# Optimization experiments

Measured on AMD Instinct MI355X. Metric: run time of the kernel, lower is better.

Reference implementation:

```python
import jax, jax.numpy as jnp
import numpy as np

NUM_TABLES = 10
EMB_DIM = 3
VOCAB = 1_000_000
N_IDX = 4_000_000
N_BAGS = 100_000


def setup_inputs() -> dict:
    key = jax.random.key(0)
    k_idx, k_off, k_w = jax.random.split(key, 3)
    eb_input = jax.random.randint(k_idx, (N_IDX,), 0, VOCAB, dtype=jnp.int64)
    # EmbeddingBag offsets: sorted, first element must be 0, values in [0, N_IDX)
    eb_offset = jnp.sort(jax.random.randint(k_off, (N_BAGS,), 0, N_IDX, dtype=jnp.int64))
    eb_offset = eb_offset.at[0].set(0)
    # torch.nn.EmbeddingBag default init: N(0, 1)
    W = jax.random.normal(k_w, (NUM_TABLES, VOCAB, EMB_DIM), dtype=jnp.float32)
    return {"eb_input": eb_input, "eb_offset": eb_offset, "W": W}


def _bag_sums(eb_input, eb_offset, W):
    # segment id for each index position: bag b covers [offset[b], offset[b+1])
    n = eb_input.shape[0]
    seg = jnp.searchsorted(eb_offset, jnp.arange(n), side="right") - 1  # [N]
    gathered = W[:, eb_input, :]  # [T, N, D] irregular gather
    # sum-pool per bag for every table
    per_bag = jax.vmap(lambda g: jax.ops.segment_sum(g, seg, num_segments=eb_offset.shape[0]))(gathered)  # [T, B, D]
    return per_bag


def reference(eb_input, eb_offset, W):
    per_bag = _bag_sums(eb_input, eb_offset, W)  # [10, B, 3]
    outs = [per_bag[i] for i in range(NUM_TABLES)]
    outs[5] = jnp.sum(outs[5], axis=1, keepdims=True)  # [B, 1]
    outs[6] = jnp.sum(outs[6], axis=1, keepdims=True)  # [B, 1]
    cat = jnp.concatenate(outs, axis=1)  # [B, 26]
    return jnp.sum(cat, axis=0)  # [26]
```

## Files before the change

### kernel.cpp

```cpp
#include <hip/hip_runtime.h>

#define VOCAB 1000000
#define NUM_TABLES 10
#define OUT_SIZE 26
#define BUCKET_BITS 12
#define BPB 4096
#define NBUCKETS 245
#define CHUNK 16384
#define MAXSRC 256
#define GSTRIDE 256
#define NGROUPS (VOCAB / 4)
#define RBLK ((NGROUPS + 255) / 256)
#define NSERIES 30


__global__ void __launch_bounds__(1024) scatter_kernel(
    const int* __restrict__ idx, int n,
    unsigned short* __restrict__ scat,
    unsigned int* __restrict__ gs32)
{
    __shared__ unsigned int lcount[256];
    __shared__ unsigned int sc[256];
    __shared__ __align__(16) unsigned short stage[CHUNK];
    const int tid = threadIdx.x;
    if (tid < 256) lcount[tid] = 0u;
    __syncthreads();

    const int4* idx4 = (const int4*)idx;
    const int n4 = n >> 2;
    const int base4 = blockIdx.x * (CHUNK / 4);
    int4 q[4];
    bool val[4];
    unsigned rank[16];
    unsigned bkt[16];
#pragma unroll
    for (int j = 0; j < 4; ++j) {
        int i4 = base4 + j * 1024 + tid;
        val[j] = (i4 < n4);
        if (val[j]) q[j] = idx4[i4];
    }
#pragma unroll
    for (int j = 0; j < 4; ++j) {
        if (val[j]) {
            unsigned v[4] = {(unsigned)q[j].x, (unsigned)q[j].y, (unsigned)q[j].z, (unsigned)q[j].w};
#pragma unroll
            for (int e = 0; e < 4; ++e) {
                bkt[j * 4 + e] = v[e] >> BUCKET_BITS;
                rank[j * 4 + e] = atomicAdd(&lcount[bkt[j * 4 + e]], 1u);
            }
        }
    }
    unsigned trank[3], tbkt[3];
    int tcnt = 0;
    if (blockIdx.x == gridDim.x - 1 && tid == 0) {
        for (int i = n4 * 4; i < n; ++i) {
            unsigned u = (unsigned)idx[i];
            tbkt[tcnt] = u >> BUCKET_BITS;
            trank[tcnt] = atomicAdd(&lcount[tbkt[tcnt]], 1u);
            ++tcnt;
        }
    }
    __syncthreads();
    unsigned cnt = 0;
    if (tid < 256) {
        cnt = (tid < NBUCKETS) ? lcount[tid] : 0u;
        sc[tid] = cnt;
    }
    __syncthreads();
#pragma unroll
    for (int off = 1; off < 256; off <<= 1) {
        unsigned v = 0, a = 0;
        if (tid < 256) {
            v = sc[tid];
            if (tid >= off) a = sc[tid - off];
        }
        __syncthreads();
        if (tid < 256) sc[tid] = v + a;
        __syncthreads();
    }
    if (tid < 256) {
        unsigned excl = sc[tid] - cnt;
        if (tid < NBUCKETS) gs32[(size_t)blockIdx.x * GSTRIDE + tid] = excl | (cnt << 16);
        lcount[tid] = excl;
    }
    __syncthreads();
#pragma unroll
    for (int j = 0; j < 4; ++j) {
        if (val[j]) {
            unsigned v[4] = {(unsigned)q[j].x, (unsigned)q[j].y, (unsigned)q[j].z, (unsigned)q[j].w};
#pragma unroll
            for (int e = 0; e < 4; ++e) {
                unsigned k = j * 4 + e;
                stage[lcount[bkt[k]] + rank[k]] = (unsigned short)(v[e] & (BPB - 1));
            }
        }
    }
    if (blockIdx.x == gridDim.x - 1 && tid == 0) {
        for (int i = 0; i < tcnt; ++i) {
            unsigned u = (unsigned)idx[n4 * 4 + i];
            stage[lcount[tbkt[i]] + trank[i]] = (unsigned short)(u & (BPB - 1));
        }
    }
    __syncthreads();
    uint4* dst = (uint4*)(scat + (size_t)blockIdx.x * CHUNK);
    const uint4* src = (const uint4*)stage;
#pragma unroll
    for (int j = 0; j < 2; ++j) dst[j * 1024 + tid] = src[j * 1024 + tid];
}

__global__ void __launch_bounds__(1024) bucket_hist_kernel(
    const unsigned short* __restrict__ scat,
    const unsigned int* __restrict__ gs32, int nsrc,
    unsigned int* __restrict__ hist)
{
    __shared__ __align__(16) unsigned int h[BPB];
    __shared__ unsigned int gcol[MAXSRC];
    const int b = blockIdx.x;
    const int tid = threadIdx.x;
    ((uint4*)h)[tid] = make_uint4(0u, 0u, 0u, 0u);
    if (tid < nsrc) gcol[tid] = gs32[(size_t)tid * GSTRIDE + b];
    __syncthreads();
    const int wave = tid >> 6, lane = tid & 63;
    for (int s = wave; s < nsrc; s += 16) {
        unsigned g32 = gcol[s];
        unsigned st = g32 & 0xffffu, c = g32 >> 16;
        const unsigned short* p = scat + (size_t)s * CHUNK + st;
        for (unsigned k = lane; k < c; k += 64)
            atomicAdd(&h[p[k]], 1u);
    }
    __syncthreads();
    int nb4 = min(BPB, VOCAB - b * BPB) >> 2;
    uint4* dst = (uint4*)(hist + (size_t)b * BPB);
    const uint4* src = (const uint4*)h;
    if (tid < nb4) dst[tid] = src[tid];
}

__device__ inline float wave_reduce(float v) {
#pragma unroll
    for (int o = 32; o > 0; o >>= 1) v += __shfl_down(v, o, 64);
    return v;
}

__global__ void __launch_bounds__(256) reduce_kernel(
    const float* __restrict__ W,
    const unsigned int* __restrict__ hist,
    float* __restrict__ partials)
{
    const int tid = threadIdx.x;
    const int g = blockIdx.x * 256 + tid;
    const int wave = tid >> 6, lane = tid & 63;
    const bool act = (g < NGROUPS);
    uint4 c4 = make_uint4(0u, 0u, 0u, 0u);
    if (act) c4 = ((const uint4*)hist)[g];
    const float c0 = (float)c4.x, c1 = (float)c4.y, c2 = (float)c4.z, c3 = (float)c4.w;
    __shared__ float sm[4][32];
#pragma unroll 2
    for (int t = 0; t < NUM_TABLES; ++t) {
        float a0 = 0.f, a1 = 0.f, a2 = 0.f;
        if (act) {
            const float4* __restrict__ W4 = (const float4*)(W + (size_t)t * VOCAB * 3);
            float4 w0 = W4[3 * g + 0];
            float4 w1 = W4[3 * g + 1];
            float4 w2 = W4[3 * g + 2];
            a0 = c0 * w0.x + c1 * w0.w + c2 * w1.z + c3 * w2.y;
            a1 = c0 * w0.y + c1 * w1.x + c2 * w1.w + c3 * w2.z;
            a2 = c0 * w0.z + c1 * w1.y + c2 * w2.x + c3 * w2.w;
        }
        a0 = wave_reduce(a0);
        a1 = wave_reduce(a1);
        a2 = wave_reduce(a2);
        if (lane == 0) {
            sm[wave][t * 3 + 0] = a0;
            sm[wave][t * 3 + 1] = a1;
            sm[wave][t * 3 + 2] = a2;
        }
    }
    __syncthreads();
    if (tid < NSERIES) {
        float v = sm[0][tid] + sm[1][tid] + sm[2][tid] + sm[3][tid];
        partials[(size_t)tid * RBLK + blockIdx.x] = v;
    }
}

__global__ void __launch_bounds__(1024) final_kernel(const float* __restrict__ partials,
                                                     float* __restrict__ out) {
    __shared__ float ts[32];
    const int tid = threadIdx.x;
    const int srs = tid >> 5;
    const int j = tid & 31;
    float v = 0.f;
    if (srs < NSERIES) {
        const float* p = partials + (size_t)srs * RBLK;
#pragma unroll
        for (int k = 0; k < (RBLK + 31) / 32; ++k) {
            int i = k * 32 + j;
            if (i < RBLK) v += p[i];
        }
    }
#pragma unroll
    for (int off = 16; off > 0; off >>= 1) v += __shfl_down(v, off);
    if (j == 0 && srs < NSERIES) ts[srs] = v;
    __syncthreads();
    if (tid < OUT_SIZE) {
        float r;
        if (tid < 15) r = ts[tid];
        else if (tid == 15) r = ts[15] + ts[16] + ts[17];
        else if (tid == 16) r = ts[18] + ts[19] + ts[20];
        else r = ts[tid + 4];
        out[tid] = r;
    }
}


__global__ void zero_kernel_fb(unsigned int* __restrict__ hist, float* __restrict__ out) {
    int i = blockIdx.x * blockDim.x + threadIdx.x;
    int n4 = VOCAB / 4;
    if (i < n4) ((uint4*)hist)[i] = make_uint4(0u, 0u, 0u, 0u);
    if (i < OUT_SIZE) out[i] = 0.0f;
}

__global__ void hist_kernel_fb(const int* __restrict__ idx, unsigned int* __restrict__ hist, int n) {
    int i = blockIdx.x * blockDim.x + threadIdx.x;
    int i4 = i * 4;
    if (i4 + 3 < n) {
        int4 v = ((const int4*)idx)[i];
        atomicAdd(&hist[v.x], 1u);
        atomicAdd(&hist[v.y], 1u);
        atomicAdd(&hist[v.z], 1u);
        atomicAdd(&hist[v.w], 1u);
    } else {
        for (int j = i4; j < n; ++j) atomicAdd(&hist[idx[j]], 1u);
    }
}

__global__ void __launch_bounds__(256) reduce_kernel_fb(const float* __restrict__ W,
                                                        const unsigned int* __restrict__ hist,
                                                        float* __restrict__ out) {
    const int t = blockIdx.x / 64;
    const int b = blockIdx.x % 64;
    const float4* __restrict__ W4 = (const float4*)(W + (size_t)t * VOCAB * 3);
    const uint4* __restrict__ h4 = (const uint4*)hist;
    const int ngroups = VOCAB / 4;
    float a0 = 0.f, a1 = 0.f, a2 = 0.f;
    const int stride = 64 * 256;
    for (int g = b * 256 + (int)threadIdx.x; g < ngroups; g += stride) {
        uint4 c4 = h4[g];
        float4 w0 = W4[3 * g + 0];
        float4 w1 = W4[3 * g + 1];
        float4 w2 = W4[3 * g + 2];
        float c0 = (float)c4.x, c1 = (float)c4.y, c2 = (float)c4.z, c3 = (float)c4.w;
        a0 += c0 * w0.x + c1 * w0.w + c2 * w1.z + c3 * w2.y;
        a1 += c0 * w0.y + c1 * w1.x + c2 * w1.w + c3 * w2.z;
        a2 += c0 * w0.z + c1 * w1.y + c2 * w2.x + c3 * w2.w;
    }
    a0 = wave_reduce(a0);
    a1 = wave_reduce(a1);
    a2 = wave_reduce(a2);
    __shared__ float s[3][4];
    int wave = threadIdx.x >> 6;
    int lane = threadIdx.x & 63;
    if (lane == 0) { s[0][wave] = a0; s[1][wave] = a1; s[2][wave] = a2; }
    __syncthreads();
    if (threadIdx.x == 0) {
        float r0 = s[0][0] + s[0][1] + s[0][2] + s[0][3];
        float r1 = s[1][0] + s[1][1] + s[1][2] + s[1][3];
        float r2 = s[2][0] + s[2][1] + s[2][2] + s[2][3];
        if (t == 5) atomicAdd(&out[15], r0 + r1 + r2);
        else if (t == 6) atomicAdd(&out[16], r0 + r1 + r2);
        else {
            int base = (t < 5) ? t * 3 : 17 + (t - 7) * 3;
            atomicAdd(&out[base + 0], r0);
            atomicAdd(&out[base + 1], r1);
            atomicAdd(&out[base + 2], r2);
        }
    }
}


extern "C" void kernel_launch(void* const* d_in, const int* in_sizes, int n_in,
                              void* d_out, int out_size, void* d_ws, size_t ws_size,
                              hipStream_t stream) {
    const int* eb_input = (const int*)d_in[0];
    const float* W = (const float*)d_in[2];
    float* out = (float*)d_out;
    int n_idx = in_sizes[0];

    const int nsrc = (n_idx + CHUNK - 1) / CHUNK;
    const size_t scat_bytes = (size_t)MAXSRC * CHUNK * 2;
    const size_t gs_off = scat_bytes;
    const size_t gs_bytes = (size_t)MAXSRC * GSTRIDE * 4;
    const size_t hist_off = gs_off + gs_bytes;
    const size_t hist_bytes = (size_t)VOCAB * 4;
    const size_t part_off = (hist_off + hist_bytes + 255) & ~(size_t)255;
    const size_t part_bytes = (size_t)NSERIES * RBLK * 4;
    const size_t need = part_off + part_bytes;

    if (nsrc <= MAXSRC && ws_size >= need) {
        unsigned short* scat = (unsigned short*)d_ws;
        unsigned int* gs32 = (unsigned int*)((char*)d_ws + gs_off);
        unsigned int* hist = (unsigned int*)((char*)d_ws + hist_off);
        float* partials = (float*)((char*)d_ws + part_off);

        scatter_kernel<<<nsrc, 1024, 0, stream>>>(eb_input, n_idx, scat, gs32);
        bucket_hist_kernel<<<NBUCKETS, 1024, 0, stream>>>(scat, gs32, nsrc, hist);
        reduce_kernel<<<RBLK, 256, 0, stream>>>(W, hist, partials);
        final_kernel<<<1, 1024, 0, stream>>>(partials, out);
    } else {
        unsigned int* hist = (unsigned int*)d_ws;
        int zblocks = (VOCAB / 4 + 255) / 256;
        zero_kernel_fb<<<zblocks, 256, 0, stream>>>(hist, out);
        int hthreads = (n_idx + 3) / 4;
        int hblocks = (hthreads + 255) / 256;
        hist_kernel_fb<<<hblocks, 256, 0, stream>>>(eb_input, hist, n_idx);
        reduce_kernel_fb<<<NUM_TABLES * 64, 256, 0, stream>>>(W, hist, out);
    }
}
```

Measured before the change: 206.0 us.

## Fuse bucket histogram and weight reduction into one kernel

Merges the per-bucket histogram kernel with the weighted reduction kernel so counts stay in shared memory instead of being written to and reread from a global histogram. This removes a global round trip of the count array and one kernel launch. In exchange, the weight streaming phase now runs on only as many blocks as there are buckets, which may lower occupancy and memory parallelism for the large W read.

New measurement: 205.4 us. About the same (-0.3%).

```diff
diff --git a/kernel.cpp b/kernel.cpp
--- a/kernel.cpp
+++ b/kernel.cpp
@@ -10,7 +10,6 @@
 #define MAXSRC 256
 #define GSTRIDE 256
 #define NGROUPS (VOCAB / 4)
-#define RBLK ((NGROUPS + 255) / 256)
 #define NSERIES 30
 
 
@@ -108,19 +107,28 @@
     for (int j = 0; j < 2; ++j) dst[j * 1024 + tid] = src[j * 1024 + tid];
 }
 
-__global__ void __launch_bounds__(1024) bucket_hist_kernel(
+__device__ inline float wave_reduce(float v) {
+#pragma unroll
+    for (int o = 32; o > 0; o >>= 1) v += __shfl_down(v, o, 64);
+    return v;
+}
+
+__global__ void __launch_bounds__(1024) bucket_reduce_kernel(
     const unsigned short* __restrict__ scat,
     const unsigned int* __restrict__ gs32, int nsrc,
-    unsigned int* __restrict__ hist)
+    const float* __restrict__ W,
+    float* __restrict__ partials)
 {
     __shared__ __align__(16) unsigned int h[BPB];
     __shared__ unsigned int gcol[MAXSRC];
+    __shared__ float sm[16][32];
     const int b = blockIdx.x;
     const int tid = threadIdx.x;
+    const int wave = tid >> 6, lane = tid & 63;
+
     ((uint4*)h)[tid] = make_uint4(0u, 0u, 0u, 0u);
     if (tid < nsrc) gcol[tid] = gs32[(size_t)tid * GSTRIDE + b];
     __syncthreads();
-    const int wave = tid >> 6, lane = tid & 63;
     for (int s = wave; s < nsrc; s += 16) {
         unsigned g32 = gcol[s];
         unsigned st = g32 & 0xffffu, c = g32 >> 16;
@@ -129,31 +137,11 @@
             atomicAdd(&h[p[k]], 1u);
     }
     __syncthreads();
-    int nb4 = min(BPB, VOCAB - b * BPB) >> 2;
-    uint4* dst = (uint4*)(hist + (size_t)b * BPB);
-    const uint4* src = (const uint4*)h;
-    if (tid < nb4) dst[tid] = src[tid];
-}
-
-__device__ inline float wave_reduce(float v) {
-#pragma unroll
-    for (int o = 32; o > 0; o >>= 1) v += __shfl_down(v, o, 64);
-    return v;
-}
-
-__global__ void __launch_bounds__(256) reduce_kernel(
-    const float* __restrict__ W,
-    const unsigned int* __restrict__ hist,
-    float* __restrict__ partials)
-{
-    const int tid = threadIdx.x;
-    const int g = blockIdx.x * 256 + tid;
-    const int wave = tid >> 6, lane = tid & 63;
+
+    const int g = b * 1024 + tid;
     const bool act = (g < NGROUPS);
-    uint4 c4 = make_uint4(0u, 0u, 0u, 0u);
-    if (act) c4 = ((const uint4*)hist)[g];
+    uint4 c4 = ((const uint4*)h)[tid];
     const float c0 = (float)c4.x, c1 = (float)c4.y, c2 = (float)c4.z, c3 = (float)c4.w;
-    __shared__ float sm[4][32];
 #pragma unroll 2
     for (int t = 0; t < NUM_TABLES; ++t) {
         float a0 = 0.f, a1 = 0.f, a2 = 0.f;
@@ -177,8 +165,10 @@
     }
     __syncthreads();
     if (tid < NSERIES) {
-        float v = sm[0][tid] + sm[1][tid] + sm[2][tid] + sm[3][tid];
-        partials[(size_t)tid * RBLK + blockIdx.x] = v;
+        float v = 0.f;
+#pragma unroll
+        for (int w = 0; w < 16; ++w) v += sm[w][tid];
+        partials[(size_t)tid * NBUCKETS + b] = v;
     }
 }
 
@@ -190,11 +180,11 @@
     const int j = tid & 31;
     float v = 0.f;
     if (srs < NSERIES) {
-        const float* p = partials + (size_t)srs * RBLK;
-#pragma unroll
-        for (int k = 0; k < (RBLK + 31) / 32; ++k) {
+        const float* p = partials + (size_t)srs * NBUCKETS;
+#pragma unroll
+        for (int k = 0; k < (NBUCKETS + 31) / 32; ++k) {
             int i = k * 32 + j;
-            if (i < RBLK) v += p[i];
+            if (i < NBUCKETS) v += p[i];
         }
     }
 #pragma unroll
@@ -289,21 +279,17 @@
     const size_t scat_bytes = (size_t)MAXSRC * CHUNK * 2;
     const size_t gs_off = scat_bytes;
     const size_t gs_bytes = (size_t)MAXSRC * GSTRIDE * 4;
-    const size_t hist_off = gs_off + gs_bytes;
-    const size_t hist_bytes = (size_t)VOCAB * 4;
-    const size_t part_off = (hist_off + hist_bytes + 255) & ~(size_t)255;
-    const size_t part_bytes = (size_t)NSERIES * RBLK * 4;
+    const size_t part_off = (gs_off + gs_bytes + 255) & ~(size_t)255;
+    const size_t part_bytes = (size_t)NSERIES * NBUCKETS * 4;
     const size_t need = part_off + part_bytes;
 
     if (nsrc <= MAXSRC && ws_size >= need) {
         unsigned short* scat = (unsigned short*)d_ws;
         unsigned int* gs32 = (unsigned int*)((char*)d_ws + gs_off);
-        unsigned int* hist = (unsigned int*)((char*)d_ws + hist_off);
         float* partials = (float*)((char*)d_ws + part_off);
 
         scatter_kernel<<<nsrc, 1024, 0, stream>>>(eb_input, n_idx, scat, gs32);
-        bucket_hist_kernel<<<NBUCKETS, 1024, 0, stream>>>(scat, gs32, nsrc, hist);
-        reduce_kernel<<<RBLK, 256, 0, stream>>>(W, hist, partials);
+        bucket_reduce_kernel<<<NBUCKETS, 1024, 0, stream>>>(scat, gs32, nsrc, W, partials);
         final_kernel<<<1, 1024, 0, stream>>>(partials, out);
     } else {
         unsigned int* hist = (unsigned int*)d_ws;
```
